# Performance work log

Measured on AMD Instinct MI355X. Metric: run time of the kernel, lower is better.

The kernel has to match this reference:

```python
import jax, jax.numpy as jnp
import numpy as np

B = 8192
D1 = 1024
D2 = 1024
H = 4096  # subnet hidden width
SCALE_LIMIT = 1.0


def _mlp(x, W1, b1, W2, b2):
    # Linear -> ReLU -> Linear
    return jnp.maximum(x @ W1 + b1, 0.0) @ W2 + b2


def setup_inputs() -> dict:
    key = jax.random.key(0)
    ks = jax.random.split(key, 17)
    inp = {"x": jax.random.normal(ks[0], (B, D1 + D2), dtype=jnp.float32)}
    # four subnets: s1,t1 map d2->d1 ; s2,t2 map d1->d2
    specs = {"s1": (D2, D1), "t1": (D2, D1), "s2": (D1, D2), "t2": (D1, D2)}
    i = 1
    for name, (din, dout) in specs.items():
        inp[f"{name}_W1"] = 0.02 * jax.random.normal(ks[i], (din, H), dtype=jnp.float32); i += 1
        inp[f"{name}_b1"] = jnp.zeros((H,), dtype=jnp.float32)
        inp[f"{name}_W2"] = 0.02 * jax.random.normal(ks[i], (H, dout), dtype=jnp.float32); i += 1
        inp[f"{name}_b2"] = jnp.zeros((dout,), dtype=jnp.float32)
    return inp


def reference(x,
              s1_W1, s1_b1, s1_W2, s1_b2,
              t1_W1, t1_b1, t1_W2, t1_b2,
              s2_W1, s2_b1, s2_W2, s2_b2,
              t2_W1, t2_b1, t2_W2, t2_b2):
    x1, x2 = x[:, :D1], x[:, D1:]
    # first half-step: update x1 conditioned on x2
    s2v = jnp.tanh(_mlp(x2, s1_W1, s1_b1, s1_W2, s1_b2)) * SCALE_LIMIT  # [B, D1]
    t2v = _mlp(x2, t1_W1, t1_b1, t1_W2, t1_b2)                          # [B, D1]
    y1 = x1 * jnp.exp(s2v) + t2v
    # second half-step: update x2 conditioned on y1
    s1v = jnp.tanh(_mlp(y1, s2_W1, s2_b1, s2_W2, s2_b2)) * SCALE_LIMIT  # [B, D2]
    t1v = _mlp(y1, t2_W1, t2_b1, t2_W2, t2_b2)                          # [B, D2]
    y2 = x2 * jnp.exp(s1v) + t1v
    y = jnp.concatenate([y1, y2], axis=1)  # [B, D1+D2]
    # exact triangular-coupling log-det (what the autograd loop computes per-sample)
    log_det = jnp.sum(s2v, axis=1) + jnp.sum(s1v, axis=1)  # [B]
    return y, log_det
```

## Files before the change

### kernel.cpp

```cpp
#include <hip/hip_runtime.h>
#include <hip/hip_bf16.h>
#include <cstdint>
#include <cstddef>

#define BDIM 8192
#define D1 1024
#define HDIM 4096

#define BM 128
#define BN 128
#define BK 64

typedef __attribute__((ext_vector_type(8))) short short8;
typedef __attribute__((ext_vector_type(4))) float f32x4;

__device__ inline void async_load16(const void* g, void* l) {
  __builtin_amdgcn_global_load_lds(
      (const __attribute__((address_space(1))) void*)g,
      (__attribute__((address_space(3))) void*)l,
      16 , 0 , 0 );
}

__device__ inline unsigned short f2bf(float f) {
  union { float f; uint32_t u; } v; v.f = f;
  uint32_t u = v.u;
  uint32_t r = u + 0x7FFFu + ((u >> 16) & 1u);
  return (unsigned short)(r >> 16);
}

__global__ __launch_bounds__(256, 2)
void gemm1_fused(const unsigned short* __restrict__ A,
                 const unsigned short* __restrict__ Bs,
                 const unsigned short* __restrict__ Bt,
                 const float* __restrict__ bias_s,
                 const float* __restrict__ bias_t,
                 unsigned short* __restrict__ Cs,
                 unsigned short* __restrict__ Ct) {
  const int K = 1024, N = 4096;
  __shared__ __align__(16) unsigned short lsA[BM * BK];
  __shared__ __align__(16) unsigned short lsS[BN * BK];
  __shared__ __align__(16) unsigned short lsT[BN * BK];

  const int tid  = threadIdx.x;
  const int wave = tid >> 6;
  const int lane = tid & 63;
  const int quad = lane >> 4;
  const int l15  = lane & 15;
  const int m0 = blockIdx.y * BM;
  const int n0 = blockIdx.x * BN;
  const int wrow = (wave >> 1) * 64;
  const int wcol = (wave & 1) * 64;

  f32x4 accS[4][4] = {};
  f32x4 accT[4][4] = {};

  for (int k0 = 0; k0 < K; k0 += BK) {
    __syncthreads();
#pragma unroll
    for (int i = 0; i < 4; ++i) {
      int s   = (wave * 4 + i) * 64 + lane;
      int row = s >> 3;
      int kg  = (s & 7) ^ (row & 7);
      async_load16(A  + (long)(m0 + row) * K + k0 + kg * 8, &lsA[(wave * 4 + i) * 512]);
      async_load16(Bs + (long)(n0 + row) * K + k0 + kg * 8, &lsS[(wave * 4 + i) * 512]);
      async_load16(Bt + (long)(n0 + row) * K + k0 + kg * 8, &lsT[(wave * 4 + i) * 512]);
    }
    __syncthreads();

#pragma unroll
    for (int ks = 0; ks < 2; ++ks) {
      short8 af[4], bs[4], bt[4];
      const int kg = ks * 4 + quad;
#pragma unroll
      for (int t = 0; t < 4; ++t) {
        int row = wrow + t * 16 + l15;
        af[t] = *(const short8*)&lsA[(row * 8 + (kg ^ (row & 7))) * 8];
        int col = wcol + t * 16 + l15;
        int pb  = col * 8 + (kg ^ (col & 7));
        bs[t] = *(const short8*)&lsS[pb * 8];
        bt[t] = *(const short8*)&lsT[pb * 8];
      }
#pragma unroll
      for (int mt = 0; mt < 4; ++mt)
#pragma unroll
        for (int nt = 0; nt < 4; ++nt) {
          accS[mt][nt] = __builtin_amdgcn_mfma_f32_16x16x32_bf16(
              af[mt], bs[nt], accS[mt][nt], 0, 0, 0);
          accT[mt][nt] = __builtin_amdgcn_mfma_f32_16x16x32_bf16(
              af[mt], bt[nt], accT[mt][nt], 0, 0, 0);
        }
    }
  }

#pragma unroll
  for (int nt = 0; nt < 4; ++nt) {
    int col = n0 + wcol + nt * 16 + l15;
    float bvs = bias_s[col], bvt = bias_t[col];
#pragma unroll
    for (int mt = 0; mt < 4; ++mt)
#pragma unroll
      for (int r = 0; r < 4; ++r) {
        long row = m0 + wrow + mt * 16 + quad * 4 + r;
        float vs = accS[mt][nt][r] + bvs;
        float vt = accT[mt][nt][r] + bvt;
        Cs[row * N + col] = f2bf(vs > 0.f ? vs : 0.f);
        Ct[row * N + col] = f2bf(vt > 0.f ? vt : 0.f);
      }
  }
}

__global__ __launch_bounds__(256, 2)
void gemm2_fused(const unsigned short* __restrict__ As,
                 const unsigned short* __restrict__ At,
                 const unsigned short* __restrict__ Bs,
                 const unsigned short* __restrict__ Bt,
                 const float* __restrict__ bias_s,
                 const float* __restrict__ bias_t,
                 const float* __restrict__ x,
                 float* __restrict__ y_out,
                 unsigned short* __restrict__ y_bf,
                 float* __restrict__ ld_out,
                 int moff, int stage) {
  const int K = 4096;
  __shared__ __align__(16) unsigned short lsAs[BM * BK];
  __shared__ __align__(16) unsigned short lsAt[BM * BK];
  __shared__ __align__(16) unsigned short lsS[BN * BK];
  __shared__ __align__(16) unsigned short lsT[BN * BK];
  __shared__ float rowsum[BM];

  const int tid  = threadIdx.x;
  const int wave = tid >> 6;
  const int lane = tid & 63;
  const int quad = lane >> 4;
  const int l15  = lane & 15;
  const int m0 = blockIdx.y * BM;
  const int n0 = blockIdx.x * BN;
  const int wrow = (wave >> 1) * 64;
  const int wcol = (wave & 1) * 64;

  f32x4 accS[4][4] = {};
  f32x4 accT[4][4] = {};

  for (int k0 = 0; k0 < K; k0 += BK) {
    __syncthreads();
#pragma unroll
    for (int i = 0; i < 4; ++i) {
      int s   = (wave * 4 + i) * 64 + lane;
      int row = s >> 3;
      int kg  = (s & 7) ^ (row & 7);
      long go = (long)row * K + k0 + kg * 8;
      async_load16(As + (long)m0 * K + go, &lsAs[(wave * 4 + i) * 512]);
      async_load16(At + (long)m0 * K + go, &lsAt[(wave * 4 + i) * 512]);
      async_load16(Bs + (long)n0 * K + go, &lsS[(wave * 4 + i) * 512]);
      async_load16(Bt + (long)n0 * K + go, &lsT[(wave * 4 + i) * 512]);
    }
    __syncthreads();

#pragma unroll
    for (int ks = 0; ks < 2; ++ks) {
      short8 as[4], at[4], bs[4], bt[4];
      const int kg = ks * 4 + quad;
#pragma unroll
      for (int t = 0; t < 4; ++t) {
        int row = wrow + t * 16 + l15;
        int pa  = row * 8 + (kg ^ (row & 7));
        as[t] = *(const short8*)&lsAs[pa * 8];
        at[t] = *(const short8*)&lsAt[pa * 8];
        int col = wcol + t * 16 + l15;
        int pb  = col * 8 + (kg ^ (col & 7));
        bs[t] = *(const short8*)&lsS[pb * 8];
        bt[t] = *(const short8*)&lsT[pb * 8];
      }
#pragma unroll
      for (int mt = 0; mt < 4; ++mt)
#pragma unroll
        for (int nt = 0; nt < 4; ++nt) {
          accS[mt][nt] = __builtin_amdgcn_mfma_f32_16x16x32_bf16(
              as[mt], bs[nt], accS[mt][nt], 0, 0, 0);
          accT[mt][nt] = __builtin_amdgcn_mfma_f32_16x16x32_bf16(
              at[mt], bt[nt], accT[mt][nt], 0, 0, 0);
        }
    }
  }

  if (tid < BM) rowsum[tid] = 0.f;
  __syncthreads();

  const int off = stage ? D1 : 0;
  float bvs[4], bvt[4];
#pragma unroll
  for (int nt = 0; nt < 4; ++nt) {
    int col = n0 + wcol + nt * 16 + l15;
    bvs[nt] = bias_s[col];
    bvt[nt] = bias_t[col];
  }
#pragma unroll
  for (int mt = 0; mt < 4; ++mt)
#pragma unroll
    for (int r = 0; r < 4; ++r) {
      long grow = (long)moff + m0 + wrow + mt * 16 + quad * 4 + r;
      float rs = 0.f;
#pragma unroll
      for (int nt = 0; nt < 4; ++nt) {
        int col = n0 + wcol + nt * 16 + l15;
        float sv = tanhf(accS[mt][nt][r] + bvs[nt]);
        rs += sv;
        float t  = accT[mt][nt][r] + bvt[nt];
        float y  = x[grow * (2 * D1) + off + col] * __expf(sv) + t;
        y_out[grow * (2 * D1) + off + col] = y;
        if (y_bf) y_bf[grow * D1 + col] = f2bf(y);
      }
#pragma unroll
      for (int o = 8; o > 0; o >>= 1) rs += __shfl_down(rs, o, 16);
      if (l15 == 0) atomicAdd(&rowsum[wrow + mt * 16 + quad * 4 + r], rs);
    }
  __syncthreads();
  if (tid < BM) atomicAdd(&ld_out[moff + m0 + tid], rowsum[tid]);
}

__global__ __launch_bounds__(256)
void transpose_cast(const float* __restrict__ in, unsigned short* __restrict__ out,
                    int R, int C) {
  __shared__ float tile[32][33];
  const int bx = blockIdx.x * 32;
  const int by = blockIdx.y * 32;
  const int tx = threadIdx.x & 31;
  const int ty = threadIdx.x >> 5;
  for (int j = ty; j < 32; j += 8)
    tile[j][tx] = in[(long)(by + j) * C + bx + tx];
  __syncthreads();
  for (int j = ty; j < 32; j += 8)
    out[(long)(bx + j) * R + by + tx] = f2bf(tile[tx][j]);
}

__global__ __launch_bounds__(256)
void cast_x2(const float* __restrict__ x, unsigned short* __restrict__ x2b) {
  long i = (long)blockIdx.x * 256 + threadIdx.x;
  long row = i >> 10, col = i & 1023;
  x2b[i] = f2bf(x[row * (2 * D1) + D1 + col]);
}

__global__ __launch_bounds__(256)
void zero_f(float* __restrict__ p, int n) {
  int i = blockIdx.x * 256 + threadIdx.x;
  if (i < n) p[i] = 0.f;
}

extern "C" void kernel_launch(void* const* d_in, const int* in_sizes, int n_in,
                              void* d_out, int out_size, void* d_ws, size_t ws_size,
                              hipStream_t stream) {
  const float* x     = (const float*)d_in[0];
  const float* s1_W1 = (const float*)d_in[1];
  const float* s1_b1 = (const float*)d_in[2];
  const float* s1_W2 = (const float*)d_in[3];
  const float* s1_b2 = (const float*)d_in[4];
  const float* t1_W1 = (const float*)d_in[5];
  const float* t1_b1 = (const float*)d_in[6];
  const float* t1_W2 = (const float*)d_in[7];
  const float* t1_b2 = (const float*)d_in[8];
  const float* s2_W1 = (const float*)d_in[9];
  const float* s2_b1 = (const float*)d_in[10];
  const float* s2_W2 = (const float*)d_in[11];
  const float* s2_b2 = (const float*)d_in[12];
  const float* t2_W1 = (const float*)d_in[13];
  const float* t2_b1 = (const float*)d_in[14];
  const float* t2_W2 = (const float*)d_in[15];
  const float* t2_b2 = (const float*)d_in[16];

  const size_t MB = 1024UL * 1024UL;
  int NC = 32;
  {
    const int cand[6] = {1, 2, 4, 8, 16, 32};
    for (int i = 0; i < 6; ++i) {
      size_t need = 80 * MB + (128 * MB) / (size_t)cand[i];
      if (need <= ws_size) { NC = cand[i]; break; }
    }
  }
  const int Mrows = BDIM / NC;

  char* ws = (char*)d_ws;
  unsigned short* w1t[4], * w2t[4];
  for (int i = 0; i < 4; ++i) {
    w1t[i] = (unsigned short*)(ws + (8 * (size_t)i) * MB);
    w2t[i] = (unsigned short*)(ws + (32 + 8 * (size_t)i) * MB);
  }
  unsigned short* xyb = (unsigned short*)(ws + 64 * MB);
  size_t hbytes = (size_t)Mrows * HDIM * 2;
  unsigned short* h_s = (unsigned short*)(ws + 80 * MB);
  unsigned short* h_t = (unsigned short*)(ws + 80 * MB + hbytes);

  float* y_out  = (float*)d_out;
  float* ld_out = (float*)d_out + (long)BDIM * (2 * D1);

  zero_f<<<(BDIM + 255) / 256, 256, 0, stream>>>(ld_out, BDIM);
  cast_x2<<<(BDIM * D1) / 256, 256, 0, stream>>>(x, xyb);
  transpose_cast<<<dim3(HDIM / 32, D1 / 32), 256, 0, stream>>>(s1_W1, w1t[0], D1, HDIM);
  transpose_cast<<<dim3(HDIM / 32, D1 / 32), 256, 0, stream>>>(t1_W1, w1t[1], D1, HDIM);
  transpose_cast<<<dim3(HDIM / 32, D1 / 32), 256, 0, stream>>>(s2_W1, w1t[2], D1, HDIM);
  transpose_cast<<<dim3(HDIM / 32, D1 / 32), 256, 0, stream>>>(t2_W1, w1t[3], D1, HDIM);
  transpose_cast<<<dim3(D1 / 32, HDIM / 32), 256, 0, stream>>>(s1_W2, w2t[0], HDIM, D1);
  transpose_cast<<<dim3(D1 / 32, HDIM / 32), 256, 0, stream>>>(t1_W2, w2t[1], HDIM, D1);
  transpose_cast<<<dim3(D1 / 32, HDIM / 32), 256, 0, stream>>>(s2_W2, w2t[2], HDIM, D1);
  transpose_cast<<<dim3(D1 / 32, HDIM / 32), 256, 0, stream>>>(t2_W2, w2t[3], HDIM, D1);

  for (int c = 0; c < NC; ++c) {
    const int moff = c * Mrows;
    unsigned short* xA = xyb + (size_t)moff * D1;

    gemm1_fused<<<dim3(HDIM / BN, Mrows / BM), 256, 0, stream>>>(
        xA, w1t[0], w1t[1], s1_b1, t1_b1, h_s, h_t);
    gemm2_fused<<<dim3(D1 / BN, Mrows / BM), 256, 0, stream>>>(
        h_s, h_t, w2t[0], w2t[1], s1_b2, t1_b2, x, y_out, xyb, ld_out, moff, 0);

    gemm1_fused<<<dim3(HDIM / BN, Mrows / BM), 256, 0, stream>>>(
        xA, w1t[2], w1t[3], s2_b1, t2_b1, h_s, h_t);
    gemm2_fused<<<dim3(D1 / BN, Mrows / BM), 256, 0, stream>>>(
        h_s, h_t, w2t[2], w2t[3], s2_b2, t2_b2, x, y_out, nullptr, ld_out, moff, 1);
  }
}
```

Before: 913.2 us.

## Split dual s/t GEMMs into single-accumulator kernels and batch weight transposes

The fused kernels kept two 4x4 accumulator sets (s and t) per wave, which needed many registers and more LDS. They are replaced by a generic single-B GEMM. The first GEMM now runs s and t as separate blockIdx.z slices. The second GEMM is split: the t branch writes its fp32 output into y_out, and a separate s kernel applies tanh/exp and adds the stored t value. This is meant to lower register and LDS pressure so more blocks fit per CU. The cost is an extra fp32 round trip through y_out and one more launch per half-step. The eight weight-transpose launches are merged into one, and zeroing ld_out is folded into the cast kernel.

```diff
diff --git a/kernel.cpp b/kernel.cpp
--- a/kernel.cpp
+++ b/kernel.cpp
@@ -29,30 +29,33 @@
 }
 
 __global__ __launch_bounds__(256, 2)
-void gemm1_fused(const unsigned short* __restrict__ A,
-                 const unsigned short* __restrict__ Bs,
-                 const unsigned short* __restrict__ Bt,
-                 const float* __restrict__ bias_s,
-                 const float* __restrict__ bias_t,
-                 unsigned short* __restrict__ Cs,
-                 unsigned short* __restrict__ Ct) {
-  const int K = 1024, N = 4096;
+void gemm_bt(const unsigned short* __restrict__ A0,
+             const unsigned short* __restrict__ A1,
+             const unsigned short* __restrict__ B0,
+             const unsigned short* __restrict__ B1,
+             const float* __restrict__ bias0,
+             const float* __restrict__ bias1,
+             void* __restrict__ C0v, void* __restrict__ C1v,
+             int M, int N, int K, int mode, int ldc, int coff, int roff) {
+  const unsigned short* A = blockIdx.z ? A1 : A0;
+  const unsigned short* B = blockIdx.z ? B1 : B0;
+  const float* bias = blockIdx.z ? bias1 : bias0;
+
   __shared__ __align__(16) unsigned short lsA[BM * BK];
-  __shared__ __align__(16) unsigned short lsS[BN * BK];
-  __shared__ __align__(16) unsigned short lsT[BN * BK];
+  __shared__ __align__(16) unsigned short lsB[BN * BK];
 
   const int tid  = threadIdx.x;
   const int wave = tid >> 6;
   const int lane = tid & 63;
   const int quad = lane >> 4;
   const int l15  = lane & 15;
+
   const int m0 = blockIdx.y * BM;
   const int n0 = blockIdx.x * BN;
   const int wrow = (wave >> 1) * 64;
   const int wcol = (wave & 1) * 64;
 
-  f32x4 accS[4][4] = {};
-  f32x4 accT[4][4] = {};
+  f32x4 acc[4][4] = {};
 
   for (int k0 = 0; k0 < K; k0 += BK) {
     __syncthreads();
@@ -61,71 +64,75 @@
       int s   = (wave * 4 + i) * 64 + lane;
       int row = s >> 3;
       int kg  = (s & 7) ^ (row & 7);
-      async_load16(A  + (long)(m0 + row) * K + k0 + kg * 8, &lsA[(wave * 4 + i) * 512]);
-      async_load16(Bs + (long)(n0 + row) * K + k0 + kg * 8, &lsS[(wave * 4 + i) * 512]);
-      async_load16(Bt + (long)(n0 + row) * K + k0 + kg * 8, &lsT[(wave * 4 + i) * 512]);
+      async_load16(A + (long)(m0 + row) * K + k0 + kg * 8, &lsA[(wave * 4 + i) * 512]);
+      async_load16(B + (long)(n0 + row) * K + k0 + kg * 8, &lsB[(wave * 4 + i) * 512]);
     }
     __syncthreads();
 
 #pragma unroll
     for (int ks = 0; ks < 2; ++ks) {
-      short8 af[4], bs[4], bt[4];
+      short8 af[4], bfr[4];
       const int kg = ks * 4 + quad;
 #pragma unroll
       for (int t = 0; t < 4; ++t) {
         int row = wrow + t * 16 + l15;
         af[t] = *(const short8*)&lsA[(row * 8 + (kg ^ (row & 7))) * 8];
         int col = wcol + t * 16 + l15;
-        int pb  = col * 8 + (kg ^ (col & 7));
-        bs[t] = *(const short8*)&lsS[pb * 8];
-        bt[t] = *(const short8*)&lsT[pb * 8];
+        bfr[t] = *(const short8*)&lsB[(col * 8 + (kg ^ (col & 7))) * 8];
       }
 #pragma unroll
       for (int mt = 0; mt < 4; ++mt)
 #pragma unroll
-        for (int nt = 0; nt < 4; ++nt) {
-          accS[mt][nt] = __builtin_amdgcn_mfma_f32_16x16x32_bf16(
-              af[mt], bs[nt], accS[mt][nt], 0, 0, 0);
-          accT[mt][nt] = __builtin_amdgcn_mfma_f32_16x16x32_bf16(
-              af[mt], bt[nt], accT[mt][nt], 0, 0, 0);
+        for (int nt = 0; nt < 4; ++nt)
+          acc[mt][nt] = __builtin_amdgcn_mfma_f32_16x16x32_bf16(
+              af[mt], bfr[nt], acc[mt][nt], 0, 0, 0);
+    }
+  }
+
+  if (mode == 0) {
+    unsigned short* C = blockIdx.z ? (unsigned short*)C1v : (unsigned short*)C0v;
+#pragma unroll
+    for (int nt = 0; nt < 4; ++nt) {
+      int col = n0 + wcol + nt * 16 + l15;
+      float bv = bias[col];
+#pragma unroll
+      for (int mt = 0; mt < 4; ++mt)
+#pragma unroll
+        for (int r = 0; r < 4; ++r) {
+          long row = m0 + wrow + mt * 16 + quad * 4 + r;
+          float v = acc[mt][nt][r] + bv;
+          C[row * ldc + col] = f2bf(v > 0.f ? v : 0.f);
         }
     }
-  }
-
-#pragma unroll
-  for (int nt = 0; nt < 4; ++nt) {
-    int col = n0 + wcol + nt * 16 + l15;
-    float bvs = bias_s[col], bvt = bias_t[col];
-#pragma unroll
-    for (int mt = 0; mt < 4; ++mt)
-#pragma unroll
-      for (int r = 0; r < 4; ++r) {
-        long row = m0 + wrow + mt * 16 + quad * 4 + r;
-        float vs = accS[mt][nt][r] + bvs;
-        float vt = accT[mt][nt][r] + bvt;
-        Cs[row * N + col] = f2bf(vs > 0.f ? vs : 0.f);
-        Ct[row * N + col] = f2bf(vt > 0.f ? vt : 0.f);
-      }
+  } else {
+    float* C = blockIdx.z ? (float*)C1v : (float*)C0v;
+#pragma unroll
+    for (int nt = 0; nt < 4; ++nt) {
+      int col = n0 + wcol + nt * 16 + l15;
+      float bv = bias[col];
+#pragma unroll
+      for (int mt = 0; mt < 4; ++mt)
+#pragma unroll
+        for (int r = 0; r < 4; ++r) {
+          long row = roff + m0 + wrow + mt * 16 + quad * 4 + r;
+          C[row * ldc + coff + col] = acc[mt][nt][r] + bv;
+        }
+    }
   }
 }
 
 __global__ __launch_bounds__(256, 2)
-void gemm2_fused(const unsigned short* __restrict__ As,
-                 const unsigned short* __restrict__ At,
-                 const unsigned short* __restrict__ Bs,
-                 const unsigned short* __restrict__ Bt,
-                 const float* __restrict__ bias_s,
-                 const float* __restrict__ bias_t,
-                 const float* __restrict__ x,
-                 float* __restrict__ y_out,
-                 unsigned short* __restrict__ y_bf,
-                 float* __restrict__ ld_out,
-                 int moff, int stage) {
+void gemm2_s(const unsigned short* __restrict__ A,
+             const unsigned short* __restrict__ B,
+             const float* __restrict__ bias,
+             const float* __restrict__ x,
+             float* __restrict__ y_out,
+             unsigned short* __restrict__ y_bf,
+             float* __restrict__ ld_out,
+             int moff, int off) {
   const int K = 4096;
-  __shared__ __align__(16) unsigned short lsAs[BM * BK];
-  __shared__ __align__(16) unsigned short lsAt[BM * BK];
-  __shared__ __align__(16) unsigned short lsS[BN * BK];
-  __shared__ __align__(16) unsigned short lsT[BN * BK];
+  __shared__ __align__(16) unsigned short lsA[BM * BK];
+  __shared__ __align__(16) unsigned short lsB[BN * BK];
   __shared__ float rowsum[BM];
 
   const int tid  = threadIdx.x;
@@ -133,13 +140,13 @@
   const int lane = tid & 63;
   const int quad = lane >> 4;
   const int l15  = lane & 15;
+
   const int m0 = blockIdx.y * BM;
   const int n0 = blockIdx.x * BN;
   const int wrow = (wave >> 1) * 64;
   const int wcol = (wave & 1) * 64;
 
-  f32x4 accS[4][4] = {};
-  f32x4 accT[4][4] = {};
+  f32x4 acc[4][4] = {};
 
   for (int k0 = 0; k0 < K; k0 += BK) {
     __syncthreads();
@@ -148,52 +155,38 @@
       int s   = (wave * 4 + i) * 64 + lane;
       int row = s >> 3;
       int kg  = (s & 7) ^ (row & 7);
-      long go = (long)row * K + k0 + kg * 8;
-      async_load16(As + (long)m0 * K + go, &lsAs[(wave * 4 + i) * 512]);
-      async_load16(At + (long)m0 * K + go, &lsAt[(wave * 4 + i) * 512]);
-      async_load16(Bs + (long)n0 * K + go, &lsS[(wave * 4 + i) * 512]);
-      async_load16(Bt + (long)n0 * K + go, &lsT[(wave * 4 + i) * 512]);
+      async_load16(A + (long)(m0 + row) * K + k0 + kg * 8, &lsA[(wave * 4 + i) * 512]);
+      async_load16(B + (long)(n0 + row) * K + k0 + kg * 8, &lsB[(wave * 4 + i) * 512]);
     }
     __syncthreads();
 
 #pragma unroll
     for (int ks = 0; ks < 2; ++ks) {
-      short8 as[4], at[4], bs[4], bt[4];
+      short8 af[4], bfr[4];
       const int kg = ks * 4 + quad;
 #pragma unroll
       for (int t = 0; t < 4; ++t) {
         int row = wrow + t * 16 + l15;
-        int pa  = row * 8 + (kg ^ (row & 7));
-        as[t] = *(const short8*)&lsAs[pa * 8];
-        at[t] = *(const short8*)&lsAt[pa * 8];
+        af[t] = *(const short8*)&lsA[(row * 8 + (kg ^ (row & 7))) * 8];
         int col = wcol + t * 16 + l15;
-        int pb  = col * 8 + (kg ^ (col & 7));
-        bs[t] = *(const short8*)&lsS[pb * 8];
-        bt[t] = *(const short8*)&lsT[pb * 8];
+        bfr[t] = *(const short8*)&lsB[(col * 8 + (kg ^ (col & 7))) * 8];
       }
 #pragma unroll
       for (int mt = 0; mt < 4; ++mt)
 #pragma unroll
-        for (int nt = 0; nt < 4; ++nt) {
-          accS[mt][nt] = __builtin_amdgcn_mfma_f32_16x16x32_bf16(
-              as[mt], bs[nt], accS[mt][nt], 0, 0, 0);
-          accT[mt][nt] = __builtin_amdgcn_mfma_f32_16x16x32_bf16(
-              at[mt], bt[nt], accT[mt][nt], 0, 0, 0);
-        }
+        for (int nt = 0; nt < 4; ++nt)
+          acc[mt][nt] = __builtin_amdgcn_mfma_f32_16x16x32_bf16(
+              af[mt], bfr[nt], acc[mt][nt], 0, 0, 0);
     }
   }
 
   if (tid < BM) rowsum[tid] = 0.f;
   __syncthreads();
 
-  const int off = stage ? D1 : 0;
-  float bvs[4], bvt[4];
-#pragma unroll
-  for (int nt = 0; nt < 4; ++nt) {
-    int col = n0 + wcol + nt * 16 + l15;
-    bvs[nt] = bias_s[col];
-    bvt[nt] = bias_t[col];
-  }
+  float bvs[4];
+#pragma unroll
+  for (int nt = 0; nt < 4; ++nt) bvs[nt] = bias[n0 + wcol + nt * 16 + l15];
+
 #pragma unroll
   for (int mt = 0; mt < 4; ++mt)
 #pragma unroll
@@ -203,11 +196,11 @@
 #pragma unroll
       for (int nt = 0; nt < 4; ++nt) {
         int col = n0 + wcol + nt * 16 + l15;
-        float sv = tanhf(accS[mt][nt][r] + bvs[nt]);
+        float sv = tanhf(acc[mt][nt][r] + bvs[nt]);
         rs += sv;
-        float t  = accT[mt][nt][r] + bvt[nt];
-        float y  = x[grow * (2 * D1) + off + col] * __expf(sv) + t;
-        y_out[grow * (2 * D1) + off + col] = y;
+        long idx = grow * (2 * D1) + off + col;
+        float y = x[idx] * __expf(sv) + y_out[idx];
+        y_out[idx] = y;
         if (y_bf) y_bf[grow * D1 + col] = f2bf(y);
       }
 #pragma unroll
@@ -219,11 +212,25 @@
 }
 
 __global__ __launch_bounds__(256)
-void transpose_cast(const float* __restrict__ in, unsigned short* __restrict__ out,
-                    int R, int C) {
+void transpose_all(const float* __restrict__ i0, const float* __restrict__ i1,
+                   const float* __restrict__ i2, const float* __restrict__ i3,
+                   const float* __restrict__ i4, const float* __restrict__ i5,
+                   const float* __restrict__ i6, const float* __restrict__ i7,
+                   unsigned short* __restrict__ o0, unsigned short* __restrict__ o1,
+                   unsigned short* __restrict__ o2, unsigned short* __restrict__ o3,
+                   unsigned short* __restrict__ o4, unsigned short* __restrict__ o5,
+                   unsigned short* __restrict__ o6, unsigned short* __restrict__ o7) {
+  const float* ins[8]  = {i0, i1, i2, i3, i4, i5, i6, i7};
+  unsigned short* outs[8] = {o0, o1, o2, o3, o4, o5, o6, o7};
+  const int z = blockIdx.z;
+  const float* in = ins[z];
+  unsigned short* out = outs[z];
+  const int R = (z < 4) ? D1 : HDIM;
+  const int C = (z < 4) ? HDIM : D1;
+  const int bx = ((z < 4) ? blockIdx.x : blockIdx.y) * 32;
+  const int by = ((z < 4) ? blockIdx.y : blockIdx.x) * 32;
+
   __shared__ float tile[32][33];
-  const int bx = blockIdx.x * 32;
-  const int by = blockIdx.y * 32;
   const int tx = threadIdx.x & 31;
   const int ty = threadIdx.x >> 5;
   for (int j = ty; j < 32; j += 8)
@@ -234,16 +241,12 @@
 }
 
 __global__ __launch_bounds__(256)
-void cast_x2(const float* __restrict__ x, unsigned short* __restrict__ x2b) {
+void cast_x2(const float* __restrict__ x, unsigned short* __restrict__ x2b,
+             float* __restrict__ ld_out) {
   long i = (long)blockIdx.x * 256 + threadIdx.x;
   long row = i >> 10, col = i & 1023;
   x2b[i] = f2bf(x[row * (2 * D1) + D1 + col]);
-}
-
-__global__ __launch_bounds__(256)
-void zero_f(float* __restrict__ p, int n) {
-  int i = blockIdx.x * 256 + threadIdx.x;
-  if (i < n) p[i] = 0.f;
+  if (i < BDIM) ld_out[i] = 0.f;
 }
 
 extern "C" void kernel_launch(void* const* d_in, const int* in_sizes, int n_in,
@@ -292,29 +295,31 @@
   float* y_out  = (float*)d_out;
   float* ld_out = (float*)d_out + (long)BDIM * (2 * D1);
 
-  zero_f<<<(BDIM + 255) / 256, 256, 0, stream>>>(ld_out, BDIM);
-  cast_x2<<<(BDIM * D1) / 256, 256, 0, stream>>>(x, xyb);
-  transpose_cast<<<dim3(HDIM / 32, D1 / 32), 256, 0, stream>>>(s1_W1, w1t[0], D1, HDIM);
-  transpose_cast<<<dim3(HDIM / 32, D1 / 32), 256, 0, stream>>>(t1_W1, w1t[1], D1, HDIM);
-  transpose_cast<<<dim3(HDIM / 32, D1 / 32), 256, 0, stream>>>(s2_W1, w1t[2], D1, HDIM);
-  transpose_cast<<<dim3(HDIM / 32, D1 / 32), 256, 0, stream>>>(t2_W1, w1t[3], D1, HDIM);
-  transpose_cast<<<dim3(D1 / 32, HDIM / 32), 256, 0, stream>>>(s1_W2, w2t[0], HDIM, D1);
-  transpose_cast<<<dim3(D1 / 32, HDIM / 32), 256, 0, stream>>>(t1_W2, w2t[1], HDIM, D1);
-  transpose_cast<<<dim3(D1 / 32, HDIM / 32), 256, 0, stream>>>(s2_W2, w2t[2], HDIM, D1);
-  transpose_cast<<<dim3(D1 / 32, HDIM / 32), 256, 0, stream>>>(t2_W2, w2t[3], HDIM, D1);
+  cast_x2<<<(BDIM * D1) / 256, 256, 0, stream>>>(x, xyb, ld_out);
+  transpose_all<<<dim3(HDIM / 32, D1 / 32, 8), 256, 0, stream>>>(
+      s1_W1, t1_W1, s2_W1, t2_W1, s1_W2, t1_W2, s2_W2, t2_W2,
+      w1t[0], w1t[1], w1t[2], w1t[3], w2t[0], w2t[1], w2t[2], w2t[3]);
 
   for (int c = 0; c < NC; ++c) {
     const int moff = c * Mrows;
     unsigned short* xA = xyb + (size_t)moff * D1;
 
-    gemm1_fused<<<dim3(HDIM / BN, Mrows / BM), 256, 0, stream>>>(
-        xA, w1t[0], w1t[1], s1_b1, t1_b1, h_s, h_t);
-    gemm2_fused<<<dim3(D1 / BN, Mrows / BM), 256, 0, stream>>>(
-        h_s, h_t, w2t[0], w2t[1], s1_b2, t1_b2, x, y_out, xyb, ld_out, moff, 0);
-
-    gemm1_fused<<<dim3(HDIM / BN, Mrows / BM), 256, 0, stream>>>(
-        xA, w1t[2], w1t[3], s2_b1, t2_b1, h_s, h_t);
-    gemm2_fused<<<dim3(D1 / BN, Mrows / BM), 256, 0, stream>>>(
-        h_s, h_t, w2t[2], w2t[3], s2_b2, t2_b2, x, y_out, nullptr, ld_out, moff, 1);
-  }
-}
+    gemm_bt<<<dim3(HDIM / BN, Mrows / BM, 2), 256, 0, stream>>>(
+        xA, xA, w1t[0], w1t[1], s1_b1, t1_b1, h_s, h_t,
+        Mrows, HDIM, D1, 0, HDIM, 0, 0);
+    gemm_bt<<<dim3(D1 / BN, Mrows / BM, 1), 256, 0, stream>>>(
+        h_t, h_t, w2t[1], w2t[1], t1_b2, t1_b2, y_out, y_out,
+        Mrows, D1, HDIM, 1, 2 * D1, 0, moff);
+    gemm2_s<<<dim3(D1 / BN, Mrows / BM), 256, 0, stream>>>(
+        h_s, w2t[0], s1_b2, x, y_out, xA, ld_out, moff, 0);
+
+    gemm_bt<<<dim3(HDIM / BN, Mrows / BM, 2), 256, 0, stream>>>(
+        xA, xA, w1t[2], w1t[3], s2_b1, t2_b1, h_s, h_t,
+        Mrows, HDIM, D1, 0, HDIM, 0, 0);
+    gemm_bt<<<dim3(D1 / BN, Mrows / BM, 1), 256, 0, stream>>>(
+        h_t, h_t, w2t[3], w2t[3], t2_b2, t2_b2, y_out, y_out,
+        Mrows, D1, HDIM, 1, 2 * D1, D1, moff);
+    gemm2_s<<<dim3(D1 / BN, Mrows / BM), 256, 0, stream>>>(
+        h_s, w2t[2], s2_b2, x, y_out, nullptr, ld_out, moff, D1);
+  }
+}
```

Result: slower. 934.9 us (+2.4%).
